# Optimization experiments

Measured on AMD Instinct MI355X. Metric: run time of the kernel, lower is better.

The kernel has to match this reference:

```python
import jax, jax.numpy as jnp
import numpy as np

N_NODES = 100000
D_IN = 256
D_OUT = 128
N_EDGES = 1600000
KEEP_PROB = 0.5  # tf.nn.dropout(input, 1 - 0.5) -> rate = 0.5


def setup_inputs() -> dict:
    key = jax.random.key(0)
    k_x, k_mask, k_w, k_row, k_col, k_ew = jax.random.split(key, 6)
    x = jax.random.normal(k_x, (N_NODES, D_IN), dtype=jnp.float32)
    # Deterministic scaled dropout keep-mask: Bernoulli(keep)/keep
    u = jax.random.uniform(k_mask, (N_NODES, D_IN), dtype=jnp.float32)
    dropout_mask = (u < KEEP_PROB).astype(jnp.float32) / KEEP_PROB
    kernel = jax.random.normal(k_w, (D_IN, D_OUT), dtype=jnp.float32) * (1.0 / np.sqrt(D_IN))
    edge_row = jax.random.randint(k_row, (N_EDGES,), 0, N_NODES, dtype=jnp.int32)
    edge_col = jax.random.randint(k_col, (N_EDGES,), 0, N_NODES, dtype=jnp.int32)
    edge_weight = jax.random.uniform(k_ew, (N_EDGES,), dtype=jnp.float32)
    return {"x": x, "dropout_mask": dropout_mask, "kernel": kernel,
            "edge_row": edge_row, "edge_col": edge_col, "edge_weight": edge_weight}


def reference(x, dropout_mask, kernel, edge_row, edge_col, edge_weight):
    # dropout (mask already scaled by 1/keep_prob)
    h = x * dropout_mask                      # [N, D_IN]
    # dense projection
    h = h @ kernel                            # [N, D_OUT]
    # sparse (COO) adjacency @ dense: out[r] += w_e * h[c] for each edge (r, c)
    msgs = edge_weight[:, None] * h[edge_col]            # [E, D_OUT]
    agg = jax.ops.segment_sum(msgs, edge_row, num_segments=N_NODES)  # [N, D_OUT]
    # act=True -> relu
    return jax.nn.relu(agg)
```

## Files before the change

kernel.cpp:

```cpp
#include <hip/hip_runtime.h>

constexpr int NN = 100000;
constexpr int DI = 256;
constexpr int DO = 128;
constexpr int NE = 1600000;

constexpr int BROWS = 128;
constexpr int NBK   = (NN + BROWS - 1) / BROWS;
constexpr int TILE  = 8192;
constexpr int CAP   = 2688;

typedef __bf16 bf16x8 __attribute__((ext_vector_type(8)));
typedef float  f32x4  __attribute__((ext_vector_type(4)));

__device__ inline unsigned short f2bf(float f) {
    union { float f; unsigned u; } v; v.f = f;
    return (unsigned short)((v.u + 0x7FFF + ((v.u >> 16) & 1)) >> 16);
}
__device__ inline float bf2f(unsigned u16) {
    union { unsigned u; float f; } v; v.u = u16 << 16;
    return v.f;
}

__global__ __launch_bounds__(256)
void wt_kernel(const float* __restrict__ W, unsigned short* __restrict__ Wt) {
    __shared__ float t[32][33];
    const int tx = threadIdx.x & 31, ty = threadIdx.x >> 5;
    const int k0 = (blockIdx.x >> 2) * 32, n0 = (blockIdx.x & 3) * 32;
#pragma unroll
    for (int i = 0; i < 32; i += 8)
        t[ty + i][tx] = W[(size_t)(k0 + ty + i) * DO + n0 + tx];
    __syncthreads();
#pragma unroll
    for (int i = 0; i < 32; i += 8)
        Wt[(size_t)(n0 + ty + i) * DI + k0 + tx] = f2bf(t[tx][ty + i]);
}

__global__ __launch_bounds__(256)
void gemm_kernel(const float* __restrict__ x, const float* __restrict__ mask,
                 const unsigned short* __restrict__ Wt,
                 unsigned short* __restrict__ h) {
    __shared__ unsigned short As[64][72];
    __shared__ unsigned short Bs[128][72];
    const int tid  = threadIdx.x;
    const int lane = tid & 63;
    const int w    = tid >> 6;
    const int m0   = blockIdx.x * 64;
    const int mw   = w * 16;
    const int l15  = lane & 15;
    const int l4   = lane >> 4;

    f32x4 acc[8];
#pragma unroll
    for (int ct = 0; ct < 8; ++ct) acc[ct] = (f32x4){0.f, 0.f, 0.f, 0.f};

    const int lr = tid >> 4;
    const int lk = (tid & 15) * 4;

    float4 xv[4], mv[4];
    const float4 z4 = make_float4(0.f, 0.f, 0.f, 0.f);

#pragma unroll
    for (int p = 0; p < 4; ++p) {
        const int r = m0 + p * 16 + lr;
        if (r < NN) {
            xv[p] = *(const float4*)(x    + (size_t)r * DI + lk);
            mv[p] = *(const float4*)(mask + (size_t)r * DI + lk);
        } else { xv[p] = z4; mv[p] = z4; }
    }

    for (int kc = 0; kc < DI; kc += 64) {
        __syncthreads();
#pragma unroll
        for (int p = 0; p < 4; ++p) {
            ushort4 pk;
            pk.x = f2bf(xv[p].x * mv[p].x); pk.y = f2bf(xv[p].y * mv[p].y);
            pk.z = f2bf(xv[p].z * mv[p].z); pk.w = f2bf(xv[p].w * mv[p].w);
            *(ushort4*)&As[p * 16 + lr][lk] = pk;
        }
        {
            const int kl = (tid & 7) * 8;
#pragma unroll
            for (int p = 0; p < 4; ++p) {
                const int n = p * 32 + (tid >> 3);
                *(uint4*)&Bs[n][kl] =
                    *(const uint4*)(Wt + (size_t)n * DI + kc + kl);
            }
        }
        if (kc + 64 < DI) {
#pragma unroll
            for (int p = 0; p < 4; ++p) {
                const int r = m0 + p * 16 + lr;
                if (r < NN) {
                    xv[p] = *(const float4*)(x    + (size_t)r * DI + kc + 64 + lk);
                    mv[p] = *(const float4*)(mask + (size_t)r * DI + kc + 64 + lk);
                } else { xv[p] = z4; mv[p] = z4; }
            }
        }
        __syncthreads();
#pragma unroll
        for (int ks = 0; ks < 2; ++ks) {
            const int ko = ks * 32 + l4 * 8;
            const bf16x8 a0 = *(const bf16x8*)&As[mw + l15][ko];
#pragma unroll
            for (int ct = 0; ct < 8; ++ct) {
                const bf16x8 b = *(const bf16x8*)&Bs[ct * 16 + l15][ko];
                acc[ct] = __builtin_amdgcn_mfma_f32_16x16x32_bf16(a0, b, acc[ct], 0, 0, 0);
            }
        }
    }
#pragma unroll
    for (int ct = 0; ct < 8; ++ct)
#pragma unroll
        for (int reg = 0; reg < 4; ++reg) {
            const int row = m0 + mw + l4 * 4 + reg;
            if (row < NN)
                h[(size_t)row * DO + ct * 16 + l15] = f2bf(acc[ct][reg]);
        }
}

__global__ __launch_bounds__(256)
void part_kernel(const int* __restrict__ erow, const int* __restrict__ ecol,
                 const float* __restrict__ ew, int* __restrict__ bcnt,
                 int2* __restrict__ csr) {
    __shared__ int cnt[NBK];
    __shared__ int base[NBK];
    const int t  = threadIdx.x;
    const int e0 = blockIdx.x * TILE;
    for (int k = t; k < NBK; k += 256) cnt[k] = 0;
    __syncthreads();
    for (int k = 0; k < TILE; k += 256) {
        const int e = e0 + k + t;
        if (e < NE) atomicAdd(&cnt[erow[e] >> 7], 1);
    }
    __syncthreads();
    for (int k = t; k < NBK; k += 256) {
        const int c = cnt[k];
        base[k] = c ? atomicAdd(&bcnt[k], c) : 0;
        cnt[k] = 0;
    }
    __syncthreads();
    for (int k = 0; k < TILE; k += 256) {
        const int e = e0 + k + t;
        if (e < NE) {
            const int row = erow[e];
            const int bk  = row >> 7;
            const int pos = atomicAdd(&cnt[bk], 1);
            int2 v;
            v.x = ((row & 127) << 17) | ecol[e];
            v.y = __float_as_int(ew[e]);
            csr[(size_t)bk * CAP + base[bk] + pos] = v;
        }
    }
}

__global__ __launch_bounds__(512)
void bgather_kernel(const unsigned short* __restrict__ h,
                    const int* __restrict__ bcnt,
                    const int2* __restrict__ csr, float* __restrict__ out) {
    __shared__ int2 se[CAP];
    __shared__ int  s_cnt[BROWS];
    __shared__ int  s_start[BROWS + 1];
    __shared__ int  wtot;
    const int b = blockIdx.x, t = threadIdx.x;
    const int n = bcnt[b];
    const int2* ebase = csr + (size_t)b * CAP;

    if (t < BROWS) s_cnt[t] = 0;
    __syncthreads();
    for (int j = t; j < n; j += 512)
        atomicAdd(&s_cnt[((unsigned)ebase[j].x) >> 17], 1);
    __syncthreads();
    const int lane = t & 63;
    int c = 0;
    if (t < BROWS) c = s_cnt[t];
    int v = c;
#pragma unroll
    for (int off = 1; off < 64; off <<= 1) {
        const int nn = __shfl_up(v, off, 64);
        if (lane >= off) v += nn;
    }
    if (t == 63) wtot = v;
    __syncthreads();
    if (t < BROWS) {
        const int excl = v - c + (t >= 64 ? wtot : 0);
        s_start[t] = excl;
        s_cnt[t]   = excl;
    }
    if (t == 0) s_start[BROWS] = n;
    __syncthreads();
    for (int j = t; j < n; j += 512) {
        const int2 cw  = ebase[j];
        const int  pos = atomicAdd(&s_cnt[((unsigned)cw.x) >> 17], 1);
        se[pos] = cw;
    }
    __syncthreads();

    const int l16 = t & 15, g = t >> 4;
    const int row0 = b * BROWS;
#pragma unroll
    for (int rp = 0; rp < 4; ++rp) {
        const int r  = rp * 32 + g;
        const int gr = row0 + r;
        const int rs = s_start[r], re = s_start[r + 1];
        float acc[8];
#pragma unroll
        for (int i = 0; i < 8; ++i) acc[i] = 0.f;
        int j = rs;
        for (; j + 2 <= re; j += 2) {
            const int2 cw0 = se[j], cw1 = se[j + 1];
            const float w0 = __int_as_float(cw0.y);
            const float w1 = __int_as_float(cw1.y);
            const uint4 q0 = *(const uint4*)(h + (size_t)(cw0.x & 0x1FFFF) * DO + l16 * 8);
            const uint4 q1 = *(const uint4*)(h + (size_t)(cw1.x & 0x1FFFF) * DO + l16 * 8);
            const unsigned* u0 = (const unsigned*)&q0;
            const unsigned* u1 = (const unsigned*)&q1;
#pragma unroll
            for (int i = 0; i < 4; ++i) {
                acc[2 * i + 0] += w0 * bf2f(u0[i] & 0xFFFF) + w1 * bf2f(u1[i] & 0xFFFF);
                acc[2 * i + 1] += w0 * bf2f(u0[i] >> 16)    + w1 * bf2f(u1[i] >> 16);
            }
        }
        if (j < re) {
            const int2 cw = se[j];
            const float w = __int_as_float(cw.y);
            const uint4 q = *(const uint4*)(h + (size_t)(cw.x & 0x1FFFF) * DO + l16 * 8);
            const unsigned* u = (const unsigned*)&q;
#pragma unroll
            for (int i = 0; i < 4; ++i) {
                acc[2 * i + 0] += w * bf2f(u[i] & 0xFFFF);
                acc[2 * i + 1] += w * bf2f(u[i] >> 16);
            }
        }
        if (gr < NN) {
            float* op = out + (size_t)gr * DO + l16 * 8;
            *(float4*)(op + 0) = make_float4(fmaxf(acc[0], 0.f), fmaxf(acc[1], 0.f),
                                             fmaxf(acc[2], 0.f), fmaxf(acc[3], 0.f));
            *(float4*)(op + 4) = make_float4(fmaxf(acc[4], 0.f), fmaxf(acc[5], 0.f),
                                             fmaxf(acc[6], 0.f), fmaxf(acc[7], 0.f));
        }
    }
}

extern "C" void kernel_launch(void* const* d_in, const int* in_sizes, int n_in,
                              void* d_out, int out_size, void* d_ws, size_t ws_size,
                              hipStream_t stream) {
    const float* x    = (const float*)d_in[0];
    const float* mask = (const float*)d_in[1];
    const float* W    = (const float*)d_in[2];
    const int*   erow = (const int*)d_in[3];
    const int*   ecol = (const int*)d_in[4];
    const float* ew   = (const float*)d_in[5];
    float* out = (float*)d_out;

    char* p = (char*)d_ws;
    unsigned short* h  = (unsigned short*)p;  p += (size_t)NN * DO * 2;
    unsigned short* Wt = (unsigned short*)p;  p += (size_t)DO * DI * 2;
    int* bcnt = (int*)p;                      p += 3200;
    int2* csr = (int2*)p;

    hipMemsetAsync(bcnt, 0, NBK * sizeof(int), stream);

    wt_kernel<<<32, 256, 0, stream>>>(W, Wt);
    gemm_kernel<<<(NN + 63) / 64, 256, 0, stream>>>(x, mask, Wt, h);
    part_kernel<<<(NE + TILE - 1) / TILE, 256, 0, stream>>>(erow, ecol, ew,
                                                            bcnt, csr);
    bgather_kernel<<<NBK, 512, 0, stream>>>(h, bcnt, csr, out);
}
```

Before: 388.6 us.

## Load GEMM operands directly into MFMA registers, drop LDS staging

```diff
diff --git a/kernel.cpp b/kernel.cpp
--- a/kernel.cpp
+++ b/kernel.cpp
@@ -36,12 +36,22 @@
         Wt[(size_t)(n0 + ty + i) * DI + k0 + tx] = f2bf(t[tx][ty + i]);
 }
 
+union BF8 { bf16x8 v; unsigned short u[8]; };
+
+__device__ inline bf16x8 mk8(const float4& a, const float4& b,
+                             const float4& ma, const float4& mb) {
+    BF8 r;
+    r.u[0] = f2bf(a.x * ma.x); r.u[1] = f2bf(a.y * ma.y);
+    r.u[2] = f2bf(a.z * ma.z); r.u[3] = f2bf(a.w * ma.w);
+    r.u[4] = f2bf(b.x * mb.x); r.u[5] = f2bf(b.y * mb.y);
+    r.u[6] = f2bf(b.z * mb.z); r.u[7] = f2bf(b.w * mb.w);
+    return r.v;
+}
+
 __global__ __launch_bounds__(256)
 void gemm_kernel(const float* __restrict__ x, const float* __restrict__ mask,
                  const unsigned short* __restrict__ Wt,
                  unsigned short* __restrict__ h) {
-    __shared__ unsigned short As[64][72];
-    __shared__ unsigned short Bs[128][72];
     const int tid  = threadIdx.x;
     const int lane = tid & 63;
     const int w    = tid >> 6;
@@ -50,65 +60,44 @@
     const int l15  = lane & 15;
     const int l4   = lane >> 4;
 
+    const int arow = m0 + mw + l15;
+    const size_t rbase = (size_t)(arow < NN ? arow : 0) * DI + l4 * 8;
+    const float4* xp = (const float4*)(x + rbase);
+    const float4* mp = (const float4*)(mask + rbase);
+
     f32x4 acc[8];
 #pragma unroll
     for (int ct = 0; ct < 8; ++ct) acc[ct] = (f32x4){0.f, 0.f, 0.f, 0.f};
 
-    const int lr = tid >> 4;
-    const int lk = (tid & 15) * 4;
-
-    float4 xv[4], mv[4];
-    const float4 z4 = make_float4(0.f, 0.f, 0.f, 0.f);
-
-#pragma unroll
-    for (int p = 0; p < 4; ++p) {
-        const int r = m0 + p * 16 + lr;
-        if (r < NN) {
-            xv[p] = *(const float4*)(x    + (size_t)r * DI + lk);
-            mv[p] = *(const float4*)(mask + (size_t)r * DI + lk);
-        } else { xv[p] = z4; mv[p] = z4; }
-    }
-
-    for (int kc = 0; kc < DI; kc += 64) {
-        __syncthreads();
-#pragma unroll
-        for (int p = 0; p < 4; ++p) {
-            ushort4 pk;
-            pk.x = f2bf(xv[p].x * mv[p].x); pk.y = f2bf(xv[p].y * mv[p].y);
-            pk.z = f2bf(xv[p].z * mv[p].z); pk.w = f2bf(xv[p].w * mv[p].w);
-            *(ushort4*)&As[p * 16 + lr][lk] = pk;
-        }
-        {
-            const int kl = (tid & 7) * 8;
-#pragma unroll
-            for (int p = 0; p < 4; ++p) {
-                const int n = p * 32 + (tid >> 3);
-                *(uint4*)&Bs[n][kl] =
-                    *(const uint4*)(Wt + (size_t)n * DI + kc + kl);
-            }
-        }
-        if (kc + 64 < DI) {
-#pragma unroll
-            for (int p = 0; p < 4; ++p) {
-                const int r = m0 + p * 16 + lr;
-                if (r < NN) {
-                    xv[p] = *(const float4*)(x    + (size_t)r * DI + kc + 64 + lk);
-                    mv[p] = *(const float4*)(mask + (size_t)r * DI + kc + 64 + lk);
-                } else { xv[p] = z4; mv[p] = z4; }
-            }
-        }
-        __syncthreads();
-#pragma unroll
-        for (int ks = 0; ks < 2; ++ks) {
-            const int ko = ks * 32 + l4 * 8;
-            const bf16x8 a0 = *(const bf16x8*)&As[mw + l15][ko];
-#pragma unroll
-            for (int ct = 0; ct < 8; ++ct) {
-                const bf16x8 b = *(const bf16x8*)&Bs[ct * 16 + l15][ko];
-                acc[ct] = __builtin_amdgcn_mfma_f32_16x16x32_bf16(a0, b, acc[ct], 0, 0, 0);
-            }
-        }
-    }
+    float4 xr[4], mr[4];
+#define LOADA(S)                                                   \
+    do {                                                           \
+        const int o = (S) * 16;                 \
+        xr[0] = xp[o + 0]; xr[1] = xp[o + 1];                      \
+        xr[2] = xp[o + 8]; xr[3] = xp[o + 9];                      \
+        mr[0] = mp[o + 0]; mr[1] = mp[o + 1];                      \
+        mr[2] = mp[o + 8]; mr[3] = mp[o + 9];                      \
+    } while (0)
+
+    LOADA(0);
+#pragma unroll
+    for (int s = 0; s < 4; ++s) {
+        const int kc = s * 64;
+        const bf16x8 a0 = mk8(xr[0], xr[1], mr[0], mr[1]);
+        const bf16x8 a1 = mk8(xr[2], xr[3], mr[2], mr[3]);
+        if (s < 3) LOADA(s + 1);
+#pragma unroll
+        for (int ct = 0; ct < 8; ++ct) {
+            const unsigned short* bp =
+                Wt + (size_t)(ct * 16 + l15) * DI + kc + l4 * 8;
+            const bf16x8 b0 = *(const bf16x8*)(bp);
+            const bf16x8 b1 = *(const bf16x8*)(bp + 32);
+            acc[ct] = __builtin_amdgcn_mfma_f32_16x16x32_bf16(a0, b0, acc[ct], 0, 0, 0);
+            acc[ct] = __builtin_amdgcn_mfma_f32_16x16x32_bf16(a1, b1, acc[ct], 0, 0, 0);
+        }
+    }
+#undef LOADA
+
 #pragma unroll
     for (int ct = 0; ct < 8; ++ct)
 #pragma unroll
```

After: 397.6 us. +2.3%, slower.

## Merge GEMM and edge partitioning into one launch with block-role dispatch

Applied to the files above, without the earlier changes.

```diff
diff --git a/kernel.cpp b/kernel.cpp
--- a/kernel.cpp
+++ b/kernel.cpp
@@ -7,8 +7,11 @@
 
 constexpr int BROWS = 128;
 constexpr int NBK   = (NN + BROWS - 1) / BROWS;
-constexpr int TILE  = 8192;
+constexpr int TILE  = 2048;
 constexpr int CAP   = 2688;
+
+constexpr int NGB = (NN + 63) / 64;
+constexpr int NPB = (NE + TILE - 1) / TILE;
 
 typedef __bf16 bf16x8 __attribute__((ext_vector_type(8)));
 typedef float  f32x4  __attribute__((ext_vector_type(4)));
@@ -37,119 +40,120 @@
 }
 
 __global__ __launch_bounds__(256)
-void gemm_kernel(const float* __restrict__ x, const float* __restrict__ mask,
-                 const unsigned short* __restrict__ Wt,
-                 unsigned short* __restrict__ h) {
-    __shared__ unsigned short As[64][72];
-    __shared__ unsigned short Bs[128][72];
-    const int tid  = threadIdx.x;
-    const int lane = tid & 63;
-    const int w    = tid >> 6;
-    const int m0   = blockIdx.x * 64;
-    const int mw   = w * 16;
-    const int l15  = lane & 15;
-    const int l4   = lane >> 4;
-
-    f32x4 acc[8];
-#pragma unroll
-    for (int ct = 0; ct < 8; ++ct) acc[ct] = (f32x4){0.f, 0.f, 0.f, 0.f};
-
-    const int lr = tid >> 4;
-    const int lk = (tid & 15) * 4;
-
-    float4 xv[4], mv[4];
-    const float4 z4 = make_float4(0.f, 0.f, 0.f, 0.f);
-
-#pragma unroll
-    for (int p = 0; p < 4; ++p) {
-        const int r = m0 + p * 16 + lr;
-        if (r < NN) {
-            xv[p] = *(const float4*)(x    + (size_t)r * DI + lk);
-            mv[p] = *(const float4*)(mask + (size_t)r * DI + lk);
-        } else { xv[p] = z4; mv[p] = z4; }
-    }
-
-    for (int kc = 0; kc < DI; kc += 64) {
+void gemm_part_kernel(const float* __restrict__ x, const float* __restrict__ mask,
+                      const unsigned short* __restrict__ Wt,
+                      unsigned short* __restrict__ h,
+                      const int* __restrict__ erow, const int* __restrict__ ecol,
+                      const float* __restrict__ ew, int* __restrict__ bcnt,
+                      int2* __restrict__ csr) {
+    __shared__ union {
+        struct { unsigned short As[64][72]; unsigned short Bs[128][72]; } g;
+        struct { int cnt[NBK]; int base[NBK]; } p;
+    } sm;
+
+    if (blockIdx.x < NGB) {
+        const int tid  = threadIdx.x;
+        const int lane = tid & 63;
+        const int w    = tid >> 6;
+        const int m0   = blockIdx.x * 64;
+        const int mw   = w * 16;
+        const int l15  = lane & 15;
+        const int l4   = lane >> 4;
+
+        f32x4 acc[8];
+#pragma unroll
+        for (int ct = 0; ct < 8; ++ct) acc[ct] = (f32x4){0.f, 0.f, 0.f, 0.f};
+
+        const int lr = tid >> 4;
+        const int lk = (tid & 15) * 4;
+
+        float4 xv[4], mv[4];
+        const float4 z4 = make_float4(0.f, 0.f, 0.f, 0.f);
+
+#pragma unroll
+        for (int p = 0; p < 4; ++p) {
+            const int r = m0 + p * 16 + lr;
+            if (r < NN) {
+                xv[p] = *(const float4*)(x    + (size_t)r * DI + lk);
+                mv[p] = *(const float4*)(mask + (size_t)r * DI + lk);
+            } else { xv[p] = z4; mv[p] = z4; }
+        }
+
+        for (int kc = 0; kc < DI; kc += 64) {
+            __syncthreads();
+#pragma unroll
+            for (int p = 0; p < 4; ++p) {
+                ushort4 pk;
+                pk.x = f2bf(xv[p].x * mv[p].x); pk.y = f2bf(xv[p].y * mv[p].y);
+                pk.z = f2bf(xv[p].z * mv[p].z); pk.w = f2bf(xv[p].w * mv[p].w);
+                *(ushort4*)&sm.g.As[p * 16 + lr][lk] = pk;
+            }
+            {
+                const int kl = (tid & 7) * 8;
+#pragma unroll
+                for (int p = 0; p < 4; ++p) {
+                    const int n = p * 32 + (tid >> 3);
+                    *(uint4*)&sm.g.Bs[n][kl] =
+                        *(const uint4*)(Wt + (size_t)n * DI + kc + kl);
+                }
+            }
+            if (kc + 64 < DI) {
+#pragma unroll
+                for (int p = 0; p < 4; ++p) {
+                    const int r = m0 + p * 16 + lr;
+                    if (r < NN) {
+                        xv[p] = *(const float4*)(x    + (size_t)r * DI + kc + 64 + lk);
+                        mv[p] = *(const float4*)(mask + (size_t)r * DI + kc + 64 + lk);
+                    } else { xv[p] = z4; mv[p] = z4; }
+                }
+            }
+            __syncthreads();
+#pragma unroll
+            for (int ks = 0; ks < 2; ++ks) {
+                const int ko = ks * 32 + l4 * 8;
+                const bf16x8 a0 = *(const bf16x8*)&sm.g.As[mw + l15][ko];
+#pragma unroll
+                for (int ct = 0; ct < 8; ++ct) {
+                    const bf16x8 b = *(const bf16x8*)&sm.g.Bs[ct * 16 + l15][ko];
+                    acc[ct] = __builtin_amdgcn_mfma_f32_16x16x32_bf16(a0, b, acc[ct], 0, 0, 0);
+                }
+            }
+        }
+#pragma unroll
+        for (int ct = 0; ct < 8; ++ct)
+#pragma unroll
+            for (int reg = 0; reg < 4; ++reg) {
+                const int row = m0 + mw + l4 * 4 + reg;
+                if (row < NN)
+                    h[(size_t)row * DO + ct * 16 + l15] = f2bf(acc[ct][reg]);
+            }
+    } else {
+        const int t  = threadIdx.x;
+        const int e0 = (blockIdx.x - NGB) * TILE;
+        for (int k = t; k < NBK; k += 256) sm.p.cnt[k] = 0;
         __syncthreads();
-#pragma unroll
-        for (int p = 0; p < 4; ++p) {
-            ushort4 pk;
-            pk.x = f2bf(xv[p].x * mv[p].x); pk.y = f2bf(xv[p].y * mv[p].y);
-            pk.z = f2bf(xv[p].z * mv[p].z); pk.w = f2bf(xv[p].w * mv[p].w);
-            *(ushort4*)&As[p * 16 + lr][lk] = pk;
-        }
-        {
-            const int kl = (tid & 7) * 8;
-#pragma unroll
-            for (int p = 0; p < 4; ++p) {
-                const int n = p * 32 + (tid >> 3);
-                *(uint4*)&Bs[n][kl] =
-                    *(const uint4*)(Wt + (size_t)n * DI + kc + kl);
-            }
-        }
-        if (kc + 64 < DI) {
-#pragma unroll
-            for (int p = 0; p < 4; ++p) {
-                const int r = m0 + p * 16 + lr;
-                if (r < NN) {
-                    xv[p] = *(const float4*)(x    + (size_t)r * DI + kc + 64 + lk);
-                    mv[p] = *(const float4*)(mask + (size_t)r * DI + kc + 64 + lk);
-                } else { xv[p] = z4; mv[p] = z4; }
-            }
+        for (int k = 0; k < TILE; k += 256) {
+            const int e = e0 + k + t;
+            if (e < NE) atomicAdd(&sm.p.cnt[erow[e] >> 7], 1);
         }
         __syncthreads();
-#pragma unroll
-        for (int ks = 0; ks < 2; ++ks) {
-            const int ko = ks * 32 + l4 * 8;
-            const bf16x8 a0 = *(const bf16x8*)&As[mw + l15][ko];
-#pragma unroll
-            for (int ct = 0; ct < 8; ++ct) {
-                const bf16x8 b = *(const bf16x8*)&Bs[ct * 16 + l15][ko];
-                acc[ct] = __builtin_amdgcn_mfma_f32_16x16x32_bf16(a0, b, acc[ct], 0, 0, 0);
-            }
-        }
-    }
-#pragma unroll
-    for (int ct = 0; ct < 8; ++ct)
-#pragma unroll
-        for (int reg = 0; reg < 4; ++reg) {
-            const int row = m0 + mw + l4 * 4 + reg;
-            if (row < NN)
-                h[(size_t)row * DO + ct * 16 + l15] = f2bf(acc[ct][reg]);
-        }
-}
-
-__global__ __launch_bounds__(256)
-void part_kernel(const int* __restrict__ erow, const int* __restrict__ ecol,
-                 const float* __restrict__ ew, int* __restrict__ bcnt,
-                 int2* __restrict__ csr) {
-    __shared__ int cnt[NBK];
-    __shared__ int base[NBK];
-    const int t  = threadIdx.x;
-    const int e0 = blockIdx.x * TILE;
-    for (int k = t; k < NBK; k += 256) cnt[k] = 0;
-    __syncthreads();
-    for (int k = 0; k < TILE; k += 256) {
-        const int e = e0 + k + t;
-        if (e < NE) atomicAdd(&cnt[erow[e] >> 7], 1);
-    }
-    __syncthreads();
-    for (int k = t; k < NBK; k += 256) {
-        const int c = cnt[k];
-        base[k] = c ? atomicAdd(&bcnt[k], c) : 0;
-        cnt[k] = 0;
-    }
-    __syncthreads();
-    for (int k = 0; k < TILE; k += 256) {
-        const int e = e0 + k + t;
-        if (e < NE) {
-            const int row = erow[e];
-            const int bk  = row >> 7;
-            const int pos = atomicAdd(&cnt[bk], 1);
-            int2 v;
-            v.x = ((row & 127) << 17) | ecol[e];
-            v.y = __float_as_int(ew[e]);
-            csr[(size_t)bk * CAP + base[bk] + pos] = v;
+        for (int k = t; k < NBK; k += 256) {
+            const int c = sm.p.cnt[k];
+            sm.p.base[k] = c ? atomicAdd(&bcnt[k], c) : 0;
+            sm.p.cnt[k] = 0;
+        }
+        __syncthreads();
+        for (int k = 0; k < TILE; k += 256) {
+            const int e = e0 + k + t;
+            if (e < NE) {
+                const int row = erow[e];
+                const int bk  = row >> 7;
+                const int pos = atomicAdd(&sm.p.cnt[bk], 1);
+                int2 v;
+                v.x = ((row & 127) << 17) | ecol[e];
+                v.y = __float_as_int(ew[e]);
+                csr[(size_t)bk * CAP + sm.p.base[bk] + pos] = v;
+            }
         }
     }
 }
@@ -262,8 +266,7 @@
     hipMemsetAsync(bcnt, 0, NBK * sizeof(int), stream);
 
     wt_kernel<<<32, 256, 0, stream>>>(W, Wt);
-    gemm_kernel<<<(NN + 63) / 64, 256, 0, stream>>>(x, mask, Wt, h);
-    part_kernel<<<(NE + TILE - 1) / TILE, 256, 0, stream>>>(erow, ecol, ew,
-                                                            bcnt, csr);
+    gemm_part_kernel<<<NGB + NPB, 256, 0, stream>>>(x, mask, Wt, h,
+                                                    erow, ecol, ew, bcnt, csr);
     bgather_kernel<<<NBK, 512, 0, stream>>>(h, bcnt, csr, out);
 }
```

Result: faster. 359.1 us, median of 2 (-7.6%).
